# Kernel tuning notes

Measured on AMD Instinct MI355X. Metric: run time of the kernel, lower is better.

## Reference

```python
import jax, jax.numpy as jnp
import numpy as np

N_NODES = 100000
N_EDGES = 1600000
NIN = 128
NHID = 128
N_GRAPHS = 1024


def _gcn_conv(x, src, dst, norm, W, b, n_nodes):
    """PyG-style GCNConv: linear (no bias) -> normalized scatter-add -> + bias."""
    xw = x @ W                                   # [N, out]
    msg = xw[src] * norm[:, None]                # gather + edge-normalize, [E', out]
    out = jax.ops.segment_sum(msg, dst, num_segments=n_nodes)
    return out + b


def _gcn_norm(edge_index, n_nodes):
    """Add self-loops and compute symmetric deg^{-1/2} normalization per edge."""
    loops = jnp.arange(n_nodes, dtype=edge_index.dtype)
    src = jnp.concatenate([edge_index[0], loops])
    dst = jnp.concatenate([edge_index[1], loops])
    deg = jax.ops.segment_sum(jnp.ones_like(dst, dtype=jnp.float32), dst,
                              num_segments=n_nodes)
    deg_isqrt = jnp.where(deg > 0, jax.lax.rsqrt(jnp.maximum(deg, 1.0)), 0.0)
    norm = deg_isqrt[src] * deg_isqrt[dst]
    return src, dst, norm


def setup_inputs() -> dict:
    key = jax.random.key(0)
    ks = jax.random.split(key, 8)
    x = jax.random.normal(ks[0], (N_NODES, NIN), dtype=jnp.float32)
    edge_index = jax.random.randint(ks[1], (2, N_EDGES), 0, N_NODES, dtype=jnp.int64)
    batch = jnp.sort(jax.random.randint(ks[2], (N_NODES,), 0, N_GRAPHS, dtype=jnp.int64))
    s_in = 1.0 / np.sqrt(NIN)
    s_h = 1.0 / np.sqrt(NHID)
    return {
        "x": x,
        "edge_index": edge_index,
        "batch": batch,
        "W1": jax.random.normal(ks[3], (NIN, NHID), dtype=jnp.float32) * s_in,
        "b1": jnp.zeros((NHID,), dtype=jnp.float32),
        "W2": jax.random.normal(ks[4], (NHID, NHID), dtype=jnp.float32) * s_h,
        "b2": jnp.zeros((NHID,), dtype=jnp.float32),
        "W3": jax.random.normal(ks[5], (NHID, NHID), dtype=jnp.float32) * s_h,
        "b3": jnp.zeros((NHID,), dtype=jnp.float32),
        "Wfc": jax.random.normal(ks[6], (NHID, 1), dtype=jnp.float32) * s_h,
        "bfc": jnp.zeros((1,), dtype=jnp.float32),
    }


def reference(x, edge_index, batch, W1, b1, W2, b2, W3, b3, Wfc, bfc):
    n_nodes = x.shape[0]
    src, dst, norm = _gcn_norm(edge_index, n_nodes)
    h = jax.nn.relu(_gcn_conv(x, src, dst, norm, W1, b1, n_nodes))
    h = jax.nn.relu(_gcn_conv(h, src, dst, norm, W2, b2, n_nodes))
    h = jax.nn.relu(_gcn_conv(h, src, dst, norm, W3, b3, n_nodes))
    # global mean pool over graphs in the batch
    sums = jax.ops.segment_sum(h, batch, num_segments=N_GRAPHS)      # [G, NHID]
    cnts = jax.ops.segment_sum(jnp.ones((n_nodes,), dtype=h.dtype), batch,
                               num_segments=N_GRAPHS)
    pooled = sums / jnp.maximum(cnts, 1.0)[:, None]
    return pooled @ Wfc + bfc                                        # [G, 1]
```

## Files before the change

kernel.cpp:

```cpp
#include <hip/hip_runtime.h>

#define N_NODES   100000
#define N_EDGES   1600000
#define NFEAT     128
#define N_GRAPHS  1024

#define BSHIFT  8
#define BNODES  256
#define NBUCK   391
#define BCAP    4608
#define SC_EDGES 8192
#define SC_EPT   32
#define SC_BLOCKS 196
#define BD_EPT   18

typedef unsigned int uint32;
typedef unsigned short ushort;
typedef __attribute__((ext_vector_type(8))) short short8;
typedef __attribute__((ext_vector_type(4))) float f32x4;

__device__ inline ushort f2b(float f) {
    uint32 x = __float_as_uint(f);
    uint32 r = x + 0x7fffu + ((x >> 16) & 1u);
    return (ushort)(r >> 16);
}
__device__ inline float blo(uint32 u) { return __uint_as_float(u << 16); }
__device__ inline float bhi(uint32 u) { return __uint_as_float(u & 0xffff0000u); }

__global__ __launch_bounds__(256) void k_scatter(const int* __restrict__ src, const int* __restrict__ dst,
                                                 int* __restrict__ cur, uint32* __restrict__ bbuf) {
    __shared__ int hist[NBUCK];
    __shared__ int lofs[NBUCK];
    __shared__ int gbase[NBUCK];
    __shared__ int wsum[4];
    __shared__ uint32 sortedP[SC_EDGES];
    __shared__ ushort sortedB[SC_EDGES];
    int t = threadIdx.x;
    int e0 = blockIdx.x * SC_EDGES;
    int total = N_EDGES - e0; if (total > SC_EDGES) total = SC_EDGES; if (total < 0) total = 0;

    for (int i = t; i < NBUCK; i += 256) hist[i] = 0;
    __syncthreads();

    uint32 val[SC_EPT];
    int    meta[SC_EPT];
    #pragma unroll
    for (int k = 0; k < SC_EPT; ++k) {
        int i = t + k * 256;
        meta[k] = -1;
        if (i < total) {
            int s = src[e0 + i], d = dst[e0 + i];
            int b = d >> BSHIFT;
            int tk = atomicAdd(&hist[b], 1);
            val[k] = ((uint32)(d & (BNODES - 1)) << 17) | (uint32)s;
            meta[k] = (b << 13) | tk;
        }
    }
    __syncthreads();
    {
        int b0 = 2 * t, b1 = 2 * t + 1;
        int h0 = (b0 < NBUCK) ? hist[b0] : 0;
        int h1 = (b1 < NBUCK) ? hist[b1] : 0;
        int ts = h0 + h1;
        int lane = t & 63, w = t >> 6;
        int inc = ts;
        #pragma unroll
        for (int d = 1; d < 64; d <<= 1) {
            int u = __shfl_up(inc, d, 64);
            if (lane >= d) inc += u;
        }
        if (lane == 63) wsum[w] = inc;
        __syncthreads();
        int wpre = 0;
        for (int i = 0; i < w; ++i) wpre += wsum[i];
        int run = wpre + inc - ts;
        if (b0 < NBUCK) {
            lofs[b0] = run;
            if (h0) gbase[b0] = atomicAdd(&cur[b0], h0);
        }
        if (b1 < NBUCK) {
            lofs[b1] = run + h0;
            if (h1) gbase[b1] = atomicAdd(&cur[b1], h1);
        }
    }
    __syncthreads();
    #pragma unroll
    for (int k = 0; k < SC_EPT; ++k) {
        if (meta[k] >= 0) {
            int b = meta[k] >> 13;
            int p = lofs[b] + (meta[k] & 0x1FFF);
            sortedP[p] = val[k];
            sortedB[p] = (ushort)b;
        }
    }
    __syncthreads();
    for (int i = t; i < total; i += 256) {
        int b = sortedB[i];
        int addr = gbase[b] + (i - lofs[b]);
        if (addr < BCAP)
            bbuf[(size_t)b * BCAP + addr] = sortedP[i];
    }
}

__global__ __launch_bounds__(256) void k_build(const uint32* __restrict__ bbuf, const int* __restrict__ cur,
                                               int* __restrict__ col, int* __restrict__ offsets,
                                               float* __restrict__ dinv) {
    int b = blockIdx.x;
    __shared__ int hist[BNODES], excl[BNODES];
    __shared__ int wsum[4], wtot[4];
    __shared__ int sorted[BCAP];
    __shared__ int sBase, sTotal;
    int t = threadIdx.x;
    {
        int pre = 0, tot = 0;
        #pragma unroll
        for (int q = 0; q < 2; ++q) {
            int i = 2 * t + q;
            if (i < NBUCK) {
                int v = cur[i]; if (v > BCAP) v = BCAP;
                tot += v;
                if (i < b) pre += v;
            }
        }
        int lane = t & 63, w = t >> 6;
        #pragma unroll
        for (int d = 32; d > 0; d >>= 1) { pre += __shfl_down(pre, d, 64); tot += __shfl_down(tot, d, 64); }
        if (lane == 0) { wsum[w] = pre; wtot[w] = tot; }
        __syncthreads();
        if (t == 0) {
            sBase = wsum[0] + wsum[1] + wsum[2] + wsum[3];
            sTotal = wtot[0] + wtot[1] + wtot[2] + wtot[3];
        }
        hist[t] = 0;
    }
    __syncthreads();
    int base = sBase;
    if (b == NBUCK - 1 && t == 0) offsets[N_NODES] = sTotal;
    int cnt = cur[b]; if (cnt > BCAP) cnt = BCAP;
    const uint32* reg = bbuf + (size_t)b * BCAP;

    uint32 val[BD_EPT];
    int    meta[BD_EPT];
    #pragma unroll
    for (int k = 0; k < BD_EPT; ++k) {
        int i = t + k * 256;
        meta[k] = -1;
        if (i < cnt) {
            uint32 p = reg[i];
            int node = p >> 17;
            int tk = atomicAdd(&hist[node], 1);
            val[k] = p & 0x1FFFF;
            meta[k] = (node << 16) | tk;
        }
    }
    __syncthreads();
    {
        int c = hist[t];
        int lane = t & 63, w = t >> 6;
        int inc = c;
        #pragma unroll
        for (int d = 1; d < 64; d <<= 1) {
            int u = __shfl_up(inc, d, 64);
            if (lane >= d) inc += u;
        }
        if (lane == 63) wsum[w] = inc;
        __syncthreads();
        int wpre = 0;
        for (int i = 0; i < w; ++i) wpre += wsum[i];
        int e = wpre + inc - c;
        excl[t] = e;
        int node = (b << BSHIFT) + t;
        if (node < N_NODES) {
            offsets[node] = base + e;
            dinv[node] = rsqrtf((float)(c + 1));
        }
    }
    __syncthreads();
    #pragma unroll
    for (int k = 0; k < BD_EPT; ++k) {
        if (meta[k] >= 0) {
            int node = meta[k] >> 16;
            sorted[excl[node] + (meta[k] & 0xFFFF)] = (int)val[k];
        }
    }
    __syncthreads();
    for (int i = t; i < cnt; i += 256) col[base + i] = sorted[i];
}

__global__ __launch_bounds__(256) void k_castw(const float* __restrict__ W1, const float* __restrict__ W2,
                                               const float* __restrict__ W3, ushort* __restrict__ WT) {
    int i = blockIdx.x * blockDim.x + threadIdx.x;
    if (i >= 3 * NFEAT * NFEAT) return;
    int l = i >> 14;
    int j = i & 16383;
    int n = j >> 7;
    int k = j & 127;
    const float* W = (l == 0) ? W1 : (l == 1) ? W2 : W3;
    WT[i] = f2b(W[k * NFEAT + n]);
}

#define WT_STRIDE 136
#define GEMM_EPILOGUE \
    __syncthreads(); \
    { \
        ushort* sC = sWT; \
        int colBase = lane & 15; \
        _Pragma("unroll") \
        for (int r = 0; r < 4; ++r) { \
            int lr = wave * 16 + kg * 4 + r; \
            _Pragma("unroll") \
            for (int nt = 0; nt < 8; ++nt) \
                sC[lr * NFEAT + nt * 16 + colBase] = f2b(acc[nt][r]); \
        } \
    } \
    __syncthreads(); \
    { \
        int rowBase = blockIdx.x * 128; \
        const float4* sC4 = (const float4*)sWT; \
        for (int i = t; i < 2048; i += 512) { \
            int row = i >> 4; \
            int gr = rowBase + row; \
            if (gr < M) ((float4*)(C + (size_t)gr * NFEAT))[i & 15] = sC4[i]; \
        } \
    }

__global__ __launch_bounds__(512) void k_gemm(const ushort* __restrict__ A,
                                              const ushort* __restrict__ WTl,
                                              ushort* __restrict__ C, int M) {
    __shared__ ushort sWT[NFEAT * WT_STRIDE];
    int t = threadIdx.x;
    for (int i = t; i < NFEAT * 16; i += 512) {
        int n = i >> 4, c = i & 15;
        *(float4*)(sWT + n * WT_STRIDE + c * 8) = ((const float4*)WTl)[i];
    }
    int wave = t >> 6, lane = t & 63;
    int m0 = blockIdx.x * 128 + wave * 16;
    int mRow = m0 + (lane & 15);
    if (mRow >= M) mRow = M - 1;
    int kg = lane >> 4;
    const short8* Ap = (const short8*)(A + (size_t)mRow * NFEAT + kg * 8);
    short8 a0 = Ap[0];
    short8 a1 = Ap[4];
    short8 a2 = Ap[8];
    short8 a3 = Ap[12];
    __syncthreads();

    f32x4 acc[8];
    #pragma unroll
    for (int nt = 0; nt < 8; ++nt) acc[nt] = (f32x4){0.f, 0.f, 0.f, 0.f};

    #pragma unroll
    for (int nt = 0; nt < 8; ++nt) {
        int n = nt * 16 + (lane & 15);
        const short8* Bp = (const short8*)(sWT + n * WT_STRIDE + kg * 8);
        short8 b0 = Bp[0];
        short8 b1 = Bp[4];
        short8 b2 = Bp[8];
        short8 b3 = Bp[12];
        acc[nt] = __builtin_amdgcn_mfma_f32_16x16x32_bf16(a0, b0, acc[nt], 0, 0, 0);
        acc[nt] = __builtin_amdgcn_mfma_f32_16x16x32_bf16(a1, b1, acc[nt], 0, 0, 0);
        acc[nt] = __builtin_amdgcn_mfma_f32_16x16x32_bf16(a2, b2, acc[nt], 0, 0, 0);
        acc[nt] = __builtin_amdgcn_mfma_f32_16x16x32_bf16(a3, b3, acc[nt], 0, 0, 0);
    }
    GEMM_EPILOGUE
}

__device__ inline short8 cvt8(const float* p) {
    float4 v0 = ((const float4*)p)[0];
    float4 v1 = ((const float4*)p)[1];
    short8 r;
    r[0] = (short)f2b(v0.x); r[1] = (short)f2b(v0.y);
    r[2] = (short)f2b(v0.z); r[3] = (short)f2b(v0.w);
    r[4] = (short)f2b(v1.x); r[5] = (short)f2b(v1.y);
    r[6] = (short)f2b(v1.z); r[7] = (short)f2b(v1.w);
    return r;
}

__global__ __launch_bounds__(512) void k_gemm_x(const float* __restrict__ A,
                                                const ushort* __restrict__ WTl,
                                                ushort* __restrict__ C, int M) {
    __shared__ ushort sWT[NFEAT * WT_STRIDE];
    int t = threadIdx.x;
    for (int i = t; i < NFEAT * 16; i += 512) {
        int n = i >> 4, c = i & 15;
        *(float4*)(sWT + n * WT_STRIDE + c * 8) = ((const float4*)WTl)[i];
    }
    int wave = t >> 6, lane = t & 63;
    int m0 = blockIdx.x * 128 + wave * 16;
    int mRow = m0 + (lane & 15);
    if (mRow >= M) mRow = M - 1;
    int kg = lane >> 4;
    const float* Ap = A + (size_t)mRow * NFEAT + kg * 8;
    short8 a0 = cvt8(Ap);
    short8 a1 = cvt8(Ap + 32);
    short8 a2 = cvt8(Ap + 64);
    short8 a3 = cvt8(Ap + 96);
    __syncthreads();

    f32x4 acc[8];
    #pragma unroll
    for (int nt = 0; nt < 8; ++nt) acc[nt] = (f32x4){0.f, 0.f, 0.f, 0.f};

    #pragma unroll
    for (int nt = 0; nt < 8; ++nt) {
        int n = nt * 16 + (lane & 15);
        const short8* Bp = (const short8*)(sWT + n * WT_STRIDE + kg * 8);
        short8 b0 = Bp[0];
        short8 b1 = Bp[4];
        short8 b2 = Bp[8];
        short8 b3 = Bp[12];
        acc[nt] = __builtin_amdgcn_mfma_f32_16x16x32_bf16(a0, b0, acc[nt], 0, 0, 0);
        acc[nt] = __builtin_amdgcn_mfma_f32_16x16x32_bf16(a1, b1, acc[nt], 0, 0, 0);
        acc[nt] = __builtin_amdgcn_mfma_f32_16x16x32_bf16(a2, b2, acc[nt], 0, 0, 0);
        acc[nt] = __builtin_amdgcn_mfma_f32_16x16x32_bf16(a3, b3, acc[nt], 0, 0, 0);
    }
    GEMM_EPILOGUE
}

#define AGG_BODY4 \
    float dn = dinv[n]; \
    int half = lane >> 4; \
    int fl = lane & 15; \
    const uint4* XW4 = (const uint4*)XWu; \
    uint4 sv = XW4[(size_t)n * 16 + fl]; \
    float ws = (half == 0) ? dn * dn : 0.f; \
    float a0 = ws * blo(sv.x), a1 = ws * bhi(sv.x); \
    float a2 = ws * blo(sv.y), a3 = ws * bhi(sv.y); \
    float a4 = ws * blo(sv.z), a5 = ws * bhi(sv.z); \
    float a6 = ws * blo(sv.w), a7 = ws * bhi(sv.w); \
    int e0 = off[n], e1 = off[n + 1]; \
    for (int base = e0; base < e1; base += 64) { \
        int len = e1 - base; if (len > 64) len = 64; \
        int cm = (lane < len) ? col[base + lane] : 0; \
        float wm = (lane < len) ? dn * dinv[cm] : 0.f; \
        int j = 0; \
        for (; j + 16 <= len; j += 16) { \
            uint4 u[4]; float w[4]; \
            _Pragma("unroll") \
            for (int p = 0; p < 4; ++p) { \
                int idx = j + 4 * p + half; \
                int cc = __shfl(cm, idx, 64); \
                w[p] = __shfl(wm, idx, 64); \
                u[p] = XW4[(size_t)cc * 16 + fl]; \
            } \
            _Pragma("unroll") \
            for (int p = 0; p < 4; ++p) { \
                a0 = fmaf(w[p], blo(u[p].x), a0); a1 = fmaf(w[p], bhi(u[p].x), a1); \
                a2 = fmaf(w[p], blo(u[p].y), a2); a3 = fmaf(w[p], bhi(u[p].y), a3); \
                a4 = fmaf(w[p], blo(u[p].z), a4); a5 = fmaf(w[p], bhi(u[p].z), a5); \
                a6 = fmaf(w[p], blo(u[p].w), a6); a7 = fmaf(w[p], bhi(u[p].w), a7); \
            } \
        } \
        for (; j < len; j += 4) { \
            int rem = len - j; \
            int idx = j + ((half < rem) ? half : 0); \
            int cc = __shfl(cm, idx, 64); \
            float ww = __shfl(wm, idx, 64); \
            if (half >= rem) ww = 0.f; \
            uint4 u = XW4[(size_t)cc * 16 + fl]; \
            a0 = fmaf(ww, blo(u.x), a0); a1 = fmaf(ww, bhi(u.x), a1); \
            a2 = fmaf(ww, blo(u.y), a2); a3 = fmaf(ww, bhi(u.y), a3); \
            a4 = fmaf(ww, blo(u.z), a4); a5 = fmaf(ww, bhi(u.z), a5); \
            a6 = fmaf(ww, blo(u.w), a6); a7 = fmaf(ww, bhi(u.w), a7); \
        } \
    } \
    a0 += __shfl_xor(a0, 32, 64); a0 += __shfl_xor(a0, 16, 64); \
    a1 += __shfl_xor(a1, 32, 64); a1 += __shfl_xor(a1, 16, 64); \
    a2 += __shfl_xor(a2, 32, 64); a2 += __shfl_xor(a2, 16, 64); \
    a3 += __shfl_xor(a3, 32, 64); a3 += __shfl_xor(a3, 16, 64); \
    a4 += __shfl_xor(a4, 32, 64); a4 += __shfl_xor(a4, 16, 64); \
    a5 += __shfl_xor(a5, 32, 64); a5 += __shfl_xor(a5, 16, 64); \
    a6 += __shfl_xor(a6, 32, 64); a6 += __shfl_xor(a6, 16, 64); \
    a7 += __shfl_xor(a7, 32, 64); a7 += __shfl_xor(a7, 16, 64);

__global__ __launch_bounds__(256) void k_agg(const uint32* __restrict__ XWu, const int* __restrict__ col,
                                             const int* __restrict__ off, const float* __restrict__ dinv,
                                             const float* __restrict__ bias, uint32* __restrict__ Hu) {
    int wid = (blockIdx.x * blockDim.x + threadIdx.x) >> 6;
    int lane = threadIdx.x & 63;
    if (wid >= N_NODES) return;
    int n = wid;
    AGG_BODY4
    if (half == 0) {
        float4 bb0 = ((const float4*)bias)[2 * fl];
        float4 bb1 = ((const float4*)bias)[2 * fl + 1];
        float r0 = fmaxf(a0 + bb0.x, 0.f), r1 = fmaxf(a1 + bb0.y, 0.f);
        float r2 = fmaxf(a2 + bb0.z, 0.f), r3 = fmaxf(a3 + bb0.w, 0.f);
        float r4 = fmaxf(a4 + bb1.x, 0.f), r5 = fmaxf(a5 + bb1.y, 0.f);
        float r6 = fmaxf(a6 + bb1.z, 0.f), r7 = fmaxf(a7 + bb1.w, 0.f);
        uint4 o;
        o.x = (uint32)f2b(r0) | ((uint32)f2b(r1) << 16);
        o.y = (uint32)f2b(r2) | ((uint32)f2b(r3) << 16);
        o.z = (uint32)f2b(r4) | ((uint32)f2b(r5) << 16);
        o.w = (uint32)f2b(r6) | ((uint32)f2b(r7) << 16);
        ((uint4*)Hu)[(size_t)n * 16 + fl] = o;
    }
}

__global__ __launch_bounds__(256) void k_agg_fc(const uint32* __restrict__ XWu, const int* __restrict__ col,
                                                const int* __restrict__ off, const float* __restrict__ dinv,
                                                const float* __restrict__ bias, const float* __restrict__ Wfc,
                                                float* __restrict__ nodeS) {
    int wid = (blockIdx.x * blockDim.x + threadIdx.x) >> 6;
    int lane = threadIdx.x & 63;
    if (wid >= N_NODES) return;
    int n = wid;
    AGG_BODY4
    float4 bb0 = ((const float4*)bias)[2 * fl];
    float4 bb1 = ((const float4*)bias)[2 * fl + 1];
    float4 wf0 = ((const float4*)Wfc)[2 * fl];
    float4 wf1 = ((const float4*)Wfc)[2 * fl + 1];
    float s = fmaxf(a0 + bb0.x, 0.f) * wf0.x + fmaxf(a1 + bb0.y, 0.f) * wf0.y
            + fmaxf(a2 + bb0.z, 0.f) * wf0.z + fmaxf(a3 + bb0.w, 0.f) * wf0.w
            + fmaxf(a4 + bb1.x, 0.f) * wf1.x + fmaxf(a5 + bb1.y, 0.f) * wf1.y
            + fmaxf(a6 + bb1.z, 0.f) * wf1.z + fmaxf(a7 + bb1.w, 0.f) * wf1.w;
    s += __shfl_xor(s, 8, 64);
    s += __shfl_xor(s, 4, 64);
    s += __shfl_xor(s, 2, 64);
    s += __shfl_xor(s, 1, 64);
    if (lane == 0) nodeS[n] = s;
}

__device__ inline int lower_bound_dev(const int* a, int n, int key) {
    int lo = 0, hi = n;
    while (lo < hi) {
        int mid = (lo + hi) >> 1;
        if (a[mid] < key) lo = mid + 1; else hi = mid;
    }
    return lo;
}

__global__ __launch_bounds__(256) void k_pool(const float* __restrict__ nodeS, const int* __restrict__ batch,
                                              const float* __restrict__ bfc, float* __restrict__ out) {
    int g = blockIdx.x;
    int t = threadIdx.x;
    int lo = lower_bound_dev(batch, N_NODES, g);
    int hi = lower_bound_dev(batch, N_NODES, g + 1);
    float s = 0.f;
    for (int i = lo + t; i < hi; i += 256) s += nodeS[i];
    for (int d = 32; d > 0; d >>= 1) s += __shfl_down(s, d, 64);
    __shared__ float ws[4];
    int lane = t & 63, w = t >> 6;
    if (lane == 0) ws[w] = s;
    __syncthreads();
    if (t == 0) {
        float tot = ws[0] + ws[1] + ws[2] + ws[3];
        float cnt = (float)(hi - lo);
        out[g] = tot / fmaxf(cnt, 1.0f) + bfc[0];
    }
}

extern "C" void kernel_launch(void* const* d_in, const int* in_sizes, int n_in,
                              void* d_out, int out_size, void* d_ws, size_t ws_size,
                              hipStream_t stream) {
    const float* x    = (const float*)d_in[0];
    const int*   ei   = (const int*)d_in[1];
    const int*   batch= (const int*)d_in[2];
    const float* W1   = (const float*)d_in[3];
    const float* b1   = (const float*)d_in[4];
    const float* W2   = (const float*)d_in[5];
    const float* b2   = (const float*)d_in[6];
    const float* W3   = (const float*)d_in[7];
    const float* b3   = (const float*)d_in[8];
    const float* Wfc  = (const float*)d_in[9];
    const float* bfc  = (const float*)d_in[10];
    float* out = (float*)d_out;

    const int* src = ei;
    const int* dst = ei + N_EDGES;

    char* p = (char*)d_ws;
    auto carve = [&](size_t bytes) { void* r = (void*)p; p += (bytes + 255) & ~(size_t)255; return r; };
    int*    cur       = (int*)   carve(sizeof(int) * NBUCK);
    uint32* bbuf      = (uint32*)carve(sizeof(uint32) * (size_t)NBUCK * BCAP);
    float*  dinv      = (float*) carve(sizeof(float) * N_NODES);
    int*    offsets   = (int*)   carve(sizeof(int) * (N_NODES + 1));
    int*    col       = (int*)   carve(sizeof(int) * N_EDGES);
    ushort* XW        = (ushort*)carve(sizeof(short) * (size_t)N_NODES * NFEAT);
    ushort* H         = (ushort*)carve(sizeof(short) * (size_t)N_NODES * NFEAT);
    ushort* WT        = (ushort*)carve(sizeof(short) * 3 * NFEAT * NFEAT);
    float*  nodeS     = (float*) carve(sizeof(float) * N_NODES);

    const int waveNodeBlocks = (N_NODES * 64 + 255) / 256;
    const int gemmBlocks = (N_NODES + 127) / 128;

    hipMemsetAsync(cur, 0, sizeof(int) * NBUCK, stream);
    k_scatter<<<SC_BLOCKS, 256, 0, stream>>>(src, dst, cur, bbuf);
    k_build<<<NBUCK, 256, 0, stream>>>(bbuf, cur, col, offsets, dinv);

    k_castw<<<(3 * NFEAT * NFEAT + 255) / 256, 256, 0, stream>>>(W1, W2, W3, WT);

    k_gemm_x<<<gemmBlocks, 512, 0, stream>>>(x, WT, XW, N_NODES);
    k_agg<<<waveNodeBlocks, 256, 0, stream>>>((const uint32*)XW, col, offsets, dinv, b1, (uint32*)H);
    k_gemm<<<gemmBlocks, 512, 0, stream>>>(H, WT + NFEAT * NFEAT, XW, N_NODES);
    k_agg<<<waveNodeBlocks, 256, 0, stream>>>((const uint32*)XW, col, offsets, dinv, b2, (uint32*)H);
    k_gemm<<<gemmBlocks, 512, 0, stream>>>(H, WT + 2 * NFEAT * NFEAT, XW, N_NODES);
    k_agg_fc<<<waveNodeBlocks, 256, 0, stream>>>((const uint32*)XW, col, offsets, dinv, b3, Wfc, nodeS);

    k_pool<<<N_GRAPHS, 256, 0, stream>>>(nodeS, batch, bfc, out);
}
```

Before: 383.5 us.

## Fuse edge scatter with first-layer GEMM into one heterogeneous launch

Merges the edge bucketing scatter kernel and the first x@W1 GEMM into a single launch: the first 391 blocks do the scatter and the remaining 782 blocks do the GEMM, sharing one shared-memory buffer. The bucket counter memset is folded into the weight cast kernel, which removes a separate memset call. The goal is to drop two launches and let the independent scatter and GEMM work overlap on the device. In exchange the scatter now runs with 512 threads per block on half as many edges each, and the union shared-memory size may cut occupancy for the GEMM blocks.

```diff
diff --git a/kernel.cpp b/kernel.cpp
--- a/kernel.cpp
+++ b/kernel.cpp
@@ -9,10 +9,13 @@
 #define BNODES  256
 #define NBUCK   391
 #define BCAP    4608
-#define SC_EDGES 8192
-#define SC_EPT   32
-#define SC_BLOCKS 196
+#define SC_EDGES 4096
+#define SC_EPT   8
+#define SC_BLOCKS 391
 #define BD_EPT   18
+
+#define WT_STRIDE 136
+#define GEMM_BLOCKS 782
 
 typedef unsigned int uint32;
 typedef unsigned short ushort;
@@ -27,78 +30,170 @@
 __device__ inline float blo(uint32 u) { return __uint_as_float(u << 16); }
 __device__ inline float bhi(uint32 u) { return __uint_as_float(u & 0xffff0000u); }
 
-__global__ __launch_bounds__(256) void k_scatter(const int* __restrict__ src, const int* __restrict__ dst,
-                                                 int* __restrict__ cur, uint32* __restrict__ bbuf) {
-    __shared__ int hist[NBUCK];
-    __shared__ int lofs[NBUCK];
-    __shared__ int gbase[NBUCK];
-    __shared__ int wsum[4];
-    __shared__ uint32 sortedP[SC_EDGES];
-    __shared__ ushort sortedB[SC_EDGES];
+__device__ inline short8 cvt8(const float* p) {
+    float4 v0 = ((const float4*)p)[0];
+    float4 v1 = ((const float4*)p)[1];
+    short8 r;
+    r[0] = (short)f2b(v0.x); r[1] = (short)f2b(v0.y);
+    r[2] = (short)f2b(v0.z); r[3] = (short)f2b(v0.w);
+    r[4] = (short)f2b(v1.x); r[5] = (short)f2b(v1.y);
+    r[6] = (short)f2b(v1.z); r[7] = (short)f2b(v1.w);
+    return r;
+}
+
+__global__ __launch_bounds__(256) void k_castw(const float* __restrict__ W1, const float* __restrict__ W2,
+                                               const float* __restrict__ W3, ushort* __restrict__ WT,
+                                               int* __restrict__ cur) {
+    int i = blockIdx.x * blockDim.x + threadIdx.x;
+    if (i < NBUCK) cur[i] = 0;
+    if (i >= 3 * NFEAT * NFEAT) return;
+    int l = i >> 14;
+    int j = i & 16383;
+    int n = j >> 7;
+    int k = j & 127;
+    const float* W = (l == 0) ? W1 : (l == 1) ? W2 : W3;
+    WT[i] = f2b(W[k * NFEAT + n]);
+}
+
+struct SMemScatter {
+    int hist[NBUCK], lofs[NBUCK], gbase[NBUCK];
+    int wsum[4];
+    uint32 sortedP[SC_EDGES];
+    ushort sortedB[SC_EDGES];
+};
+
+__global__ __launch_bounds__(512) void k_phase1(const int* __restrict__ src, const int* __restrict__ dst,
+                                                int* __restrict__ cur, uint32* __restrict__ bbuf,
+                                                const float* __restrict__ A, const ushort* __restrict__ WTl,
+                                                ushort* __restrict__ C, int M) {
+    __shared__ __align__(16) char smem[NFEAT * WT_STRIDE * 2];
     int t = threadIdx.x;
-    int e0 = blockIdx.x * SC_EDGES;
-    int total = N_EDGES - e0; if (total > SC_EDGES) total = SC_EDGES; if (total < 0) total = 0;
-
-    for (int i = t; i < NBUCK; i += 256) hist[i] = 0;
-    __syncthreads();
-
-    uint32 val[SC_EPT];
-    int    meta[SC_EPT];
-    #pragma unroll
-    for (int k = 0; k < SC_EPT; ++k) {
-        int i = t + k * 256;
-        meta[k] = -1;
-        if (i < total) {
-            int s = src[e0 + i], d = dst[e0 + i];
-            int b = d >> BSHIFT;
-            int tk = atomicAdd(&hist[b], 1);
-            val[k] = ((uint32)(d & (BNODES - 1)) << 17) | (uint32)s;
-            meta[k] = (b << 13) | tk;
-        }
-    }
-    __syncthreads();
-    {
-        int b0 = 2 * t, b1 = 2 * t + 1;
-        int h0 = (b0 < NBUCK) ? hist[b0] : 0;
-        int h1 = (b1 < NBUCK) ? hist[b1] : 0;
-        int ts = h0 + h1;
-        int lane = t & 63, w = t >> 6;
-        int inc = ts;
-        #pragma unroll
-        for (int d = 1; d < 64; d <<= 1) {
-            int u = __shfl_up(inc, d, 64);
-            if (lane >= d) inc += u;
-        }
-        if (lane == 63) wsum[w] = inc;
-        __syncthreads();
-        int wpre = 0;
-        for (int i = 0; i < w; ++i) wpre += wsum[i];
-        int run = wpre + inc - ts;
-        if (b0 < NBUCK) {
-            lofs[b0] = run;
-            if (h0) gbase[b0] = atomicAdd(&cur[b0], h0);
-        }
-        if (b1 < NBUCK) {
-            lofs[b1] = run + h0;
-            if (h1) gbase[b1] = atomicAdd(&cur[b1], h1);
-        }
-    }
-    __syncthreads();
-    #pragma unroll
-    for (int k = 0; k < SC_EPT; ++k) {
-        if (meta[k] >= 0) {
-            int b = meta[k] >> 13;
-            int p = lofs[b] + (meta[k] & 0x1FFF);
-            sortedP[p] = val[k];
-            sortedB[p] = (ushort)b;
-        }
-    }
-    __syncthreads();
-    for (int i = t; i < total; i += 256) {
-        int b = sortedB[i];
-        int addr = gbase[b] + (i - lofs[b]);
-        if (addr < BCAP)
-            bbuf[(size_t)b * BCAP + addr] = sortedP[i];
+    if (blockIdx.x < SC_BLOCKS) {
+        SMemScatter& S = *(SMemScatter*)smem;
+        int e0 = blockIdx.x * SC_EDGES;
+        int total = N_EDGES - e0; if (total > SC_EDGES) total = SC_EDGES; if (total < 0) total = 0;
+        for (int i = t; i < NBUCK; i += 512) S.hist[i] = 0;
+        __syncthreads();
+        uint32 val[SC_EPT];
+        int    meta[SC_EPT];
+        #pragma unroll
+        for (int k = 0; k < SC_EPT; ++k) {
+            int i = t + k * 512;
+            meta[k] = -1;
+            if (i < total) {
+                int s = src[e0 + i], d = dst[e0 + i];
+                int b = d >> BSHIFT;
+                int tk = atomicAdd(&S.hist[b], 1);
+                val[k] = ((uint32)(d & (BNODES - 1)) << 17) | (uint32)s;
+                meta[k] = (b << 13) | tk;
+            }
+        }
+        __syncthreads();
+        int inc = 0, ts = 0, h0 = 0;
+        if (t < 256) {
+            int b0 = 2 * t, b1 = 2 * t + 1;
+            h0 = (b0 < NBUCK) ? S.hist[b0] : 0;
+            int h1 = (b1 < NBUCK) ? S.hist[b1] : 0;
+            ts = h0 + h1;
+            int lane = t & 63;
+            inc = ts;
+            #pragma unroll
+            for (int d = 1; d < 64; d <<= 1) {
+                int u = __shfl_up(inc, d, 64);
+                if (lane >= d) inc += u;
+            }
+            if (lane == 63) S.wsum[t >> 6] = inc;
+        }
+        __syncthreads();
+        if (t < 256) {
+            int w = t >> 6;
+            int wpre = 0;
+            for (int i = 0; i < w; ++i) wpre += S.wsum[i];
+            int run = wpre + inc - ts;
+            int b0 = 2 * t, b1 = 2 * t + 1;
+            int h1 = ts - h0;
+            if (b0 < NBUCK) {
+                S.lofs[b0] = run;
+                if (h0) S.gbase[b0] = atomicAdd(&cur[b0], h0);
+            }
+            if (b1 < NBUCK) {
+                S.lofs[b1] = run + h0;
+                if (h1) S.gbase[b1] = atomicAdd(&cur[b1], h1);
+            }
+        }
+        __syncthreads();
+        #pragma unroll
+        for (int k = 0; k < SC_EPT; ++k) {
+            if (meta[k] >= 0) {
+                int b = meta[k] >> 13;
+                int p = S.lofs[b] + (meta[k] & 0x1FFF);
+                S.sortedP[p] = val[k];
+                S.sortedB[p] = (ushort)b;
+            }
+        }
+        __syncthreads();
+        for (int i = t; i < total; i += 512) {
+            int b = S.sortedB[i];
+            int addr = S.gbase[b] + (i - S.lofs[b]);
+            if (addr < BCAP)
+                bbuf[(size_t)b * BCAP + addr] = S.sortedP[i];
+        }
+    } else {
+        ushort* sWT = (ushort*)smem;
+        int gb = blockIdx.x - SC_BLOCKS;
+        for (int i = t; i < NFEAT * 16; i += 512) {
+            int n = i >> 4, c = i & 15;
+            *(float4*)(sWT + n * WT_STRIDE + c * 8) = ((const float4*)WTl)[i];
+        }
+        int wave = t >> 6, lane = t & 63;
+        int m0 = gb * 128 + wave * 16;
+        int mRow = m0 + (lane & 15);
+        if (mRow >= M) mRow = M - 1;
+        int kg = lane >> 4;
+        const float* Ap = A + (size_t)mRow * NFEAT + kg * 8;
+        short8 a0 = cvt8(Ap);
+        short8 a1 = cvt8(Ap + 32);
+        short8 a2 = cvt8(Ap + 64);
+        short8 a3 = cvt8(Ap + 96);
+        __syncthreads();
+
+        f32x4 acc[8];
+        #pragma unroll
+        for (int nt = 0; nt < 8; ++nt) acc[nt] = (f32x4){0.f, 0.f, 0.f, 0.f};
+        #pragma unroll
+        for (int nt = 0; nt < 8; ++nt) {
+            int n = nt * 16 + (lane & 15);
+            const short8* Bp = (const short8*)(sWT + n * WT_STRIDE + kg * 8);
+            short8 b0 = Bp[0];
+            short8 b1 = Bp[4];
+            short8 b2 = Bp[8];
+            short8 b3 = Bp[12];
+            acc[nt] = __builtin_amdgcn_mfma_f32_16x16x32_bf16(a0, b0, acc[nt], 0, 0, 0);
+            acc[nt] = __builtin_amdgcn_mfma_f32_16x16x32_bf16(a1, b1, acc[nt], 0, 0, 0);
+            acc[nt] = __builtin_amdgcn_mfma_f32_16x16x32_bf16(a2, b2, acc[nt], 0, 0, 0);
+            acc[nt] = __builtin_amdgcn_mfma_f32_16x16x32_bf16(a3, b3, acc[nt], 0, 0, 0);
+        }
+        __syncthreads();
+        {
+            int colBase = lane & 15;
+            #pragma unroll
+            for (int r = 0; r < 4; ++r) {
+                int lr = wave * 16 + kg * 4 + r;
+                #pragma unroll
+                for (int nt = 0; nt < 8; ++nt)
+                    sWT[lr * NFEAT + nt * 16 + colBase] = f2b(acc[nt][r]);
+            }
+        }
+        __syncthreads();
+        {
+            int rowBase = gb * 128;
+            const float4* sC4 = (const float4*)sWT;
+            for (int i = t; i < 2048; i += 512) {
+                int row = i >> 4;
+                int gr = rowBase + row;
+                if (gr < M) ((float4*)(C + (size_t)gr * NFEAT))[i & 15] = sC4[i];
+            }
+        }
     }
 }
 
@@ -187,43 +282,6 @@
     for (int i = t; i < cnt; i += 256) col[base + i] = sorted[i];
 }
 
-__global__ __launch_bounds__(256) void k_castw(const float* __restrict__ W1, const float* __restrict__ W2,
-                                               const float* __restrict__ W3, ushort* __restrict__ WT) {
-    int i = blockIdx.x * blockDim.x + threadIdx.x;
-    if (i >= 3 * NFEAT * NFEAT) return;
-    int l = i >> 14;
-    int j = i & 16383;
-    int n = j >> 7;
-    int k = j & 127;
-    const float* W = (l == 0) ? W1 : (l == 1) ? W2 : W3;
-    WT[i] = f2b(W[k * NFEAT + n]);
-}
-
-#define WT_STRIDE 136
-#define GEMM_EPILOGUE \
-    __syncthreads(); \
-    { \
-        ushort* sC = sWT; \
-        int colBase = lane & 15; \
-        _Pragma("unroll") \
-        for (int r = 0; r < 4; ++r) { \
-            int lr = wave * 16 + kg * 4 + r; \
-            _Pragma("unroll") \
-            for (int nt = 0; nt < 8; ++nt) \
-                sC[lr * NFEAT + nt * 16 + colBase] = f2b(acc[nt][r]); \
-        } \
-    } \
-    __syncthreads(); \
-    { \
-        int rowBase = blockIdx.x * 128; \
-        const float4* sC4 = (const float4*)sWT; \
-        for (int i = t; i < 2048; i += 512) { \
-            int row = i >> 4; \
-            int gr = rowBase + row; \
-            if (gr < M) ((float4*)(C + (size_t)gr * NFEAT))[i & 15] = sC4[i]; \
-        } \
-    }
-
 __global__ __launch_bounds__(512) void k_gemm(const ushort* __restrict__ A,
                                               const ushort* __restrict__ WTl,
                                               ushort* __restrict__ C, int M) {
@@ -248,7 +306,6 @@
     f32x4 acc[8];
     #pragma unroll
     for (int nt = 0; nt < 8; ++nt) acc[nt] = (f32x4){0.f, 0.f, 0.f, 0.f};
-
     #pragma unroll
     for (int nt = 0; nt < 8; ++nt) {
         int n = nt * 16 + (lane & 15);
@@ -262,59 +319,27 @@
         acc[nt] = __builtin_amdgcn_mfma_f32_16x16x32_bf16(a2, b2, acc[nt], 0, 0, 0);
         acc[nt] = __builtin_amdgcn_mfma_f32_16x16x32_bf16(a3, b3, acc[nt], 0, 0, 0);
     }
-    GEMM_EPILOGUE
-}
-
-__device__ inline short8 cvt8(const float* p) {
-    float4 v0 = ((const float4*)p)[0];
-    float4 v1 = ((const float4*)p)[1];
-    short8 r;
-    r[0] = (short)f2b(v0.x); r[1] = (short)f2b(v0.y);
-    r[2] = (short)f2b(v0.z); r[3] = (short)f2b(v0.w);
-    r[4] = (short)f2b(v1.x); r[5] = (short)f2b(v1.y);
-    r[6] = (short)f2b(v1.z); r[7] = (short)f2b(v1.w);
-    return r;
-}
-
-__global__ __launch_bounds__(512) void k_gemm_x(const float* __restrict__ A,
-                                                const ushort* __restrict__ WTl,
-                                                ushort* __restrict__ C, int M) {
-    __shared__ ushort sWT[NFEAT * WT_STRIDE];
-    int t = threadIdx.x;
-    for (int i = t; i < NFEAT * 16; i += 512) {
-        int n = i >> 4, c = i & 15;
-        *(float4*)(sWT + n * WT_STRIDE + c * 8) = ((const float4*)WTl)[i];
-    }
-    int wave = t >> 6, lane = t & 63;
-    int m0 = blockIdx.x * 128 + wave * 16;
-    int mRow = m0 + (lane & 15);
-    if (mRow >= M) mRow = M - 1;
-    int kg = lane >> 4;
-    const float* Ap = A + (size_t)mRow * NFEAT + kg * 8;
-    short8 a0 = cvt8(Ap);
-    short8 a1 = cvt8(Ap + 32);
-    short8 a2 = cvt8(Ap + 64);
-    short8 a3 = cvt8(Ap + 96);
-    __syncthreads();
-
-    f32x4 acc[8];
-    #pragma unroll
-    for (int nt = 0; nt < 8; ++nt) acc[nt] = (f32x4){0.f, 0.f, 0.f, 0.f};
-
-    #pragma unroll
-    for (int nt = 0; nt < 8; ++nt) {
-        int n = nt * 16 + (lane & 15);
-        const short8* Bp = (const short8*)(sWT + n * WT_STRIDE + kg * 8);
-        short8 b0 = Bp[0];
-        short8 b1 = Bp[4];
-        short8 b2 = Bp[8];
-        short8 b3 = Bp[12];
-        acc[nt] = __builtin_amdgcn_mfma_f32_16x16x32_bf16(a0, b0, acc[nt], 0, 0, 0);
-        acc[nt] = __builtin_amdgcn_mfma_f32_16x16x32_bf16(a1, b1, acc[nt], 0, 0, 0);
-        acc[nt] = __builtin_amdgcn_mfma_f32_16x16x32_bf16(a2, b2, acc[nt], 0, 0, 0);
-        acc[nt] = __builtin_amdgcn_mfma_f32_16x16x32_bf16(a3, b3, acc[nt], 0, 0, 0);
-    }
-    GEMM_EPILOGUE
+    __syncthreads();
+    {
+        int colBase = lane & 15;
+        #pragma unroll
+        for (int r = 0; r < 4; ++r) {
+            int lr = wave * 16 + kg * 4 + r;
+            #pragma unroll
+            for (int nt = 0; nt < 8; ++nt)
+                sWT[lr * NFEAT + nt * 16 + colBase] = f2b(acc[nt][r]);
+        }
+    }
+    __syncthreads();
+    {
+        int rowBase = blockIdx.x * 128;
+        const float4* sC4 = (const float4*)sWT;
+        for (int i = t; i < 2048; i += 512) {
+            int row = i >> 4;
+            int gr = rowBase + row;
+            if (gr < M) ((float4*)(C + (size_t)gr * NFEAT))[i & 15] = sC4[i];
+        }
+    }
 }
 
 #define AGG_BODY4 \
@@ -482,19 +507,15 @@
     float*  nodeS     = (float*) carve(sizeof(float) * N_NODES);
 
     const int waveNodeBlocks = (N_NODES * 64 + 255) / 256;
-    const int gemmBlocks = (N_NODES + 127) / 128;
-
-    hipMemsetAsync(cur, 0, sizeof(int) * NBUCK, stream);
-    k_scatter<<<SC_BLOCKS, 256, 0, stream>>>(src, dst, cur, bbuf);
+
+    k_castw<<<(3 * NFEAT * NFEAT + 255) / 256, 256, 0, stream>>>(W1, W2, W3, WT, cur);
+    k_phase1<<<SC_BLOCKS + GEMM_BLOCKS, 512, 0, stream>>>(src, dst, cur, bbuf, x, WT, XW, N_NODES);
     k_build<<<NBUCK, 256, 0, stream>>>(bbuf, cur, col, offsets, dinv);
 
-    k_castw<<<(3 * NFEAT * NFEAT + 255) / 256, 256, 0, stream>>>(W1, W2, W3, WT);
-
-    k_gemm_x<<<gemmBlocks, 512, 0, stream>>>(x, WT, XW, N_NODES);
     k_agg<<<waveNodeBlocks, 256, 0, stream>>>((const uint32*)XW, col, offsets, dinv, b1, (uint32*)H);
-    k_gemm<<<gemmBlocks, 512, 0, stream>>>(H, WT + NFEAT * NFEAT, XW, N_NODES);
+    k_gemm<<<GEMM_BLOCKS, 512, 0, stream>>>(H, WT + NFEAT * NFEAT, XW, N_NODES);
     k_agg<<<waveNodeBlocks, 256, 0, stream>>>((const uint32*)XW, col, offsets, dinv, b2, (uint32*)H);
-    k_gemm<<<gemmBlocks, 512, 0, stream>>>(H, WT + 2 * NFEAT * NFEAT, XW, N_NODES);
+    k_gemm<<<GEMM_BLOCKS, 512, 0, stream>>>(H, WT + 2 * NFEAT * NFEAT, XW, N_NODES);
     k_agg_fc<<<waveNodeBlocks, 256, 0, stream>>>((const uint32*)XW, col, offsets, dinv, b3, Wfc, nodeS);
 
     k_pool<<<N_GRAPHS, 256, 0, stream>>>(nodeS, batch, bfc, out);
```

New measurement: 372.5 us (median of 2 runs). 1.03x faster.
